# Kernel tuning notes

Hardware: AMD Instinct MI355X
Metric: run time of the kernel (lower is better)

## Reference

```python
import jax, jax.numpy as jnp
import numpy as np

N, F, H, C = 4096, 512, 8, 128
LEAKY_ALPHA = 0.2
MASK_VAL = -10e9  # spektral uses -10e9 * (1 - A)


def setup_inputs() -> dict:
    key = jax.random.key(0)
    k1, k2, k3, k4, k5 = jax.random.split(key, 5)
    X = jax.random.normal(k1, (N, F), dtype=jnp.float32)
    # sparse-ish binary adjacency with self loops (dense layout as the layer expects)
    A = (jax.random.uniform(k2, (N, N)) < 0.01).astype(jnp.float32)
    A = jnp.maximum(A, jnp.eye(N, dtype=jnp.float32))
    W = jax.random.normal(k3, (H, F, C), dtype=jnp.float32) * (1.0 / np.sqrt(F))
    a_self = jax.random.normal(k4, (H, C), dtype=jnp.float32) * (1.0 / np.sqrt(C))
    a_neigh = jax.random.normal(k5, (H, C), dtype=jnp.float32) * (1.0 / np.sqrt(C))
    bias = jnp.zeros((H, C), dtype=jnp.float32)
    return {"X": X, "A": A, "W": W, "a_self": a_self, "a_neigh": a_neigh, "bias": bias}


def reference(X, A, W, a_self, a_neigh, bias):
    # per-head feature projection: [H, N, C]
    feats = jnp.einsum("nf,hfc->hnc", X, W)
    # attention scores e_ij = LeakyReLU(a_self . h_i + a_neigh . h_j)
    s_self = jnp.einsum("hnc,hc->hn", feats, a_self)    # [H, N]
    s_neigh = jnp.einsum("hnc,hc->hn", feats, a_neigh)  # [H, N]
    dense = s_self[:, :, None] + s_neigh[:, None, :]    # [H, N, N]
    dense = jnp.where(dense > 0, dense, LEAKY_ALPHA * dense)
    # adjacency mask then row softmax (dropout_rate=0 -> identity)
    dense = dense + MASK_VAL * (1.0 - A)[None, :, :]
    coef = jax.nn.softmax(dense, axis=-1)               # [H, N, N]
    out = jnp.einsum("hnm,hmc->hnc", coef, feats)       # [H, N, C]
    out = out + bias[:, None, :]
    # concat heads: [N, H*C]
    out = jnp.transpose(out, (1, 0, 2)).reshape(N, H * C)
    return jax.nn.relu(out)
```

## Files before the change

kernel.cpp:

```cpp
#include <hip/hip_runtime.h>
#include <hip/hip_bf16.h>

#define GN 4096
#define GF 512
#define GH 8
#define GC 128
#define CAP 256
#define LCAP 128
#define XS 72

typedef __hip_bfloat16 bf16;
typedef unsigned short u16;
typedef unsigned int u32;
typedef __attribute__((ext_vector_type(8))) short bf16x8;
typedef __attribute__((ext_vector_type(4))) float f32x4;

static __device__ inline u16 f2u16(float x) {
    union { bf16 b; u16 u; } cv;
    cv.b = __float2bfloat16(x);
    return cv.u;
}

static __device__ inline float bf2f(short s) {
    return __uint_as_float((u32)(u16)s << 16);
}

__global__ __launch_bounds__(256) void prep_csr_kernel(
    const float* __restrict__ A, const float* __restrict__ X,
    const float* __restrict__ W, int* __restrict__ deg,
    u16* __restrict__ lists, u16* __restrict__ Xb, u16* __restrict__ WT)
{
    __shared__ u16 sT[16][520];
    int tid = threadIdx.x;
    int b   = blockIdx.x;

    if (b < 1024) {
        size_t idx = ((size_t)b * 256 + tid) * 8;
        float4 v0 = *(const float4*)(X + idx);
        float4 v1 = *(const float4*)(X + idx + 4);
        u16 o[8] = {f2u16(v0.x), f2u16(v0.y), f2u16(v0.z), f2u16(v0.w),
                    f2u16(v1.x), f2u16(v1.y), f2u16(v1.z), f2u16(v1.w)};
        *(bf16x8*)(Xb + idx) = *(bf16x8*)o;
        return;
    }
    if (b < 1088) {
        int wb = b - 1024;
        int h  = wb >> 3;
        int s16 = (wb & 7) * 16;
        const float* Wh = W + (size_t)h * GF * GC;
        for (int pass = 0; pass < 8; ++pass) {
            int k  = pass * 64 + (tid >> 2);
            int n4 = tid & 3;
            float4 v = *(const float4*)&Wh[(size_t)k * GC + s16 + n4 * 4];
            sT[n4 * 4 + 0][k] = f2u16(v.x);
            sT[n4 * 4 + 1][k] = f2u16(v.y);
            sT[n4 * 4 + 2][k] = f2u16(v.z);
            sT[n4 * 4 + 3][k] = f2u16(v.w);
        }
        __syncthreads();
        int n = tid >> 4, seg = tid & 15;
        u16* dst = WT + ((size_t)h * GC + s16 + n) * GF + seg * 32;
#pragma unroll
        for (int s = 0; s < 4; ++s)
            *(bf16x8*)(dst + s * 8) = *(const bf16x8*)&sT[n][seg * 32 + s * 8];
        return;
    }

    int i    = b - 1088;
    int lane = tid & 63;
    int* cnt = (int*)&sT[0][0];
    if (tid == 0) *cnt = 0;
    __syncthreads();

    u16* row = lists + (size_t)i * CAP;
    const float4* Arow = (const float4*)(A + (size_t)i * GN);
    unsigned long long ltmask = (lane == 63) ? ~0ull >> 1
                                             : (1ull << lane) - 1;

    float4 av[4];
#pragma unroll
    for (int it = 0; it < 4; ++it) av[it] = Arow[it * 256 + tid];

#pragma unroll
    for (int it = 0; it < 4; ++it) {
        float4 a = av[it];
        int j = (it * 256 + tid) * 4;
        bool f0 = a.x > 0.5f, f1 = a.y > 0.5f, f2 = a.z > 0.5f, f3 = a.w > 0.5f;
        unsigned long long m0 = __ballot(f0);
        unsigned long long m1 = __ballot(f1);
        unsigned long long m2 = __ballot(f2);
        unsigned long long m3 = __ballot(f3);
        int c0 = __popcll(m0), c1 = __popcll(m1), c2 = __popcll(m2);
        int tot = c0 + c1 + c2 + __popcll(m3);
        int base = 0;
        if (lane == 0 && tot) base = atomicAdd(cnt, tot);
        base = __shfl(base, 0);
        if (tot) {
            if (f0) {
                int s = base + __popcll(m0 & ltmask);
                if (s < CAP) row[s] = (u16)j;
            }
            if (f1) {
                int s = base + c0 + __popcll(m1 & ltmask);
                if (s < CAP) row[s] = (u16)(j + 1);
            }
            if (f2) {
                int s = base + c0 + c1 + __popcll(m2 & ltmask);
                if (s < CAP) row[s] = (u16)(j + 2);
            }
            if (f3) {
                int s = base + c0 + c1 + c2 + __popcll(m3 & ltmask);
                if (s < CAP) row[s] = (u16)(j + 3);
            }
        }
    }
    __syncthreads();
    if (tid == 0) deg[i] = *cnt < CAP ? *cnt : CAP;
}

__global__ __launch_bounds__(256) void feats_kernel(
    const u16* __restrict__ Xb, const u16* __restrict__ WT,
    const float* __restrict__ a_self, const float* __restrict__ a_neigh,
    u16* __restrict__ featsb, float* __restrict__ ssT,
    float* __restrict__ snT)
{
    __shared__ u16 sX[64 * XS];
    __shared__ u16 sW[128 * XS];

    int h   = blockIdx.x >> 6;
    int n0  = (blockIdx.x & 63) << 6;
    int tid = threadIdx.x;
    int lane = tid & 63, wv = tid >> 6;
    int lm = lane & 15, q = lane >> 4;

    const u16* Xp = Xb + (size_t)n0 * GF;
    const u16* Wp = WT + (size_t)h * GC * GF;

    uint4 xr[2], wr[4];

#define ISSUE_TILE(K0)                                                        \
    {                                                                         \
        _Pragma("unroll")                                                     \
        for (int it = 0; it < 2; ++it) {                                      \
            int idx = it * 256 + tid, row = idx >> 3, c = idx & 7;            \
            xr[it] = *(const uint4*)&Xp[(size_t)row * GF + (K0) + c * 8];     \
        }                                                                     \
        _Pragma("unroll")                                                     \
        for (int it = 0; it < 4; ++it) {                                      \
            int idx = it * 256 + tid, row = idx >> 3, c = idx & 7;            \
            wr[it] = *(const uint4*)&Wp[(size_t)row * GF + (K0) + c * 8];     \
        }                                                                     \
    }

#define STORE_TILE()                                                          \
    {                                                                         \
        _Pragma("unroll")                                                     \
        for (int it = 0; it < 2; ++it) {                                      \
            int idx = it * 256 + tid, row = idx >> 3, c = idx & 7;            \
            *(uint4*)&sX[row * XS + c * 8] = xr[it];                          \
        }                                                                     \
        _Pragma("unroll")                                                     \
        for (int it = 0; it < 4; ++it) {                                      \
            int idx = it * 256 + tid, row = idx >> 3, c = idx & 7;            \
            *(uint4*)&sW[row * XS + c * 8] = wr[it];                          \
        }                                                                     \
    }

    f32x4 acc[8];
#pragma unroll
    for (int nt = 0; nt < 8; ++nt) acc[nt] = (f32x4){0.f, 0.f, 0.f, 0.f};

    ISSUE_TILE(0)
    STORE_TILE()

    for (int k0 = 0; k0 < GF; k0 += 64) {
        __syncthreads();
        if (k0 + 64 < GF) ISSUE_TILE(k0 + 64)

#pragma unroll
        for (int ks = 0; ks < 64; ks += 32) {
            bf16x8 af = *(const bf16x8*)&sX[(wv * 16 + lm) * XS + ks + q * 8];
            bf16x8 bfr[8];
#pragma unroll
            for (int nt = 0; nt < 8; ++nt)
                bfr[nt] = *(const bf16x8*)&sW[(nt * 16 + lm) * XS + ks + q * 8];
#pragma unroll
            for (int nt = 0; nt < 8; ++nt)
                acc[nt] = __builtin_amdgcn_mfma_f32_16x16x32_bf16(
                    af, bfr[nt], acc[nt], 0, 0, 0);
        }
        __syncthreads();
        if (k0 + 64 < GF) STORE_TILE()
    }
#undef ISSUE_TILE
#undef STORE_TILE

    float aS[8], aN[8];
#pragma unroll
    for (int nt = 0; nt < 8; ++nt) {
        aS[nt] = a_self[h * GC + nt * 16 + lm];
        aN[nt] = a_neigh[h * GC + nt * 16 + lm];
    }
    float vs[4] = {0.f, 0.f, 0.f, 0.f};
    float vn[4] = {0.f, 0.f, 0.f, 0.f};
    int rbase = n0 + wv * 16 + q * 4;
    u16* fB = featsb + (size_t)(h >> 1) * GN * 256 + (h & 1) * 128;
#pragma unroll
    for (int nt = 0; nt < 8; ++nt) {
        f32x4 v = acc[nt];
        int col = nt * 16 + lm;
#pragma unroll
        for (int r = 0; r < 4; ++r) {
            fB[(size_t)(rbase + r) * 256 + col] = f2u16(v[r]);
            vs[r] += v[r] * aS[nt];
            vn[r] += v[r] * aN[nt];
        }
    }
#pragma unroll
    for (int r = 0; r < 4; ++r) {
        for (int off = 1; off < 16; off <<= 1) {
            vs[r] += __shfl_xor(vs[r], off);
            vn[r] += __shfl_xor(vn[r], off);
        }
        if (lm == 0) {
            ssT[(rbase + r) * GH + h] = vs[r];
            snT[(rbase + r) * GH + h] = vn[r];
        }
    }
}

__global__ __launch_bounds__(256) void attn_kernel(
    const int* __restrict__ deg, const u16* __restrict__ lists,
    const float* __restrict__ bias, const u16* __restrict__ featsb,
    const float* __restrict__ ssT, const float* __restrict__ snT,
    float* __restrict__ out)
{
    int tid  = threadIdx.x;
    int wv   = tid >> 6, lane = tid & 63;
    int bid  = blockIdx.x;
    int r8   = bid & 7;
    int hp   = r8 >> 1;
    int i    = (bid >> 3) * 8 + (r8 & 1) * 4 + wv;

    __shared__ float4 pjbuf[4][LCAP];
    float4* pj = pjbuf[wv];

    int M = deg[i];
    M = M < LCAP ? M : LCAP;
    const u16* row = lists + (size_t)i * CAP;

    float2 ssv = *(const float2*)&ssT[(size_t)i * GH + hp * 2];

    int ka = lane, kb = lane + 64;
    int ja = 0, jb = 0;
    float e0a = -1e30f, e1a = -1e30f, e0b = -1e30f, e1b = -1e30f;
    if (ka < M) {
        ja = row[ka];
        float2 sn = *(const float2*)&snT[(size_t)ja * GH + hp * 2];
        e0a = ssv.x + sn.x; e0a = e0a > 0.f ? e0a : 0.2f * e0a;
        e1a = ssv.y + sn.y; e1a = e1a > 0.f ? e1a : 0.2f * e1a;
    }
    if (kb < M) {
        jb = row[kb];
        float2 sn = *(const float2*)&snT[(size_t)jb * GH + hp * 2];
        e0b = ssv.x + sn.x; e0b = e0b > 0.f ? e0b : 0.2f * e0b;
        e1b = ssv.y + sn.y; e1b = e1b > 0.f ? e1b : 0.2f * e1b;
    }
    float m0 = fmaxf(e0a, e0b), m1 = fmaxf(e1a, e1b);
#pragma unroll
    for (int off = 32; off > 0; off >>= 1) {
        m0 = fmaxf(m0, __shfl_xor(m0, off));
        m1 = fmaxf(m1, __shfl_xor(m1, off));
    }

    float s0 = 0.f, s1 = 0.f;
    if (ka < M) {
        float p0 = __expf(e0a - m0), p1 = __expf(e1a - m1);
        pj[ka] = make_float4(p0, p1, __int_as_float(ja), 0.f);
        s0 += p0; s1 += p1;
    }
    if (kb < M) {
        float p0 = __expf(e0b - m0), p1 = __expf(e1b - m1);
        pj[kb] = make_float4(p0, p1, __int_as_float(jb), 0.f);
        s0 += p0; s1 += p1;
    }
#pragma unroll
    for (int off = 32; off > 0; off >>= 1) {
        s0 += __shfl_xor(s0, off);
        s1 += __shfl_xor(s1, off);
    }

    int par = lane >> 5;
    int cl  = lane & 31;
    float inv = (cl < 16) ? 1.f / s0 : 1.f / s1;

    const u16* fb = featsb + (size_t)hp * GN * 256 + cl * 8;
    float a0 = 0.f, a1 = 0.f, a2 = 0.f, a3 = 0.f;
    float a4 = 0.f, a5 = 0.f, a6 = 0.f, a7 = 0.f;

#define ACCUM(Q, WW)                                                          \
    {                                                                         \
        a0 += (WW) * bf2f((Q)[0]); a1 += (WW) * bf2f((Q)[1]);                 \
        a2 += (WW) * bf2f((Q)[2]); a3 += (WW) * bf2f((Q)[3]);                 \
        a4 += (WW) * bf2f((Q)[4]); a5 += (WW) * bf2f((Q)[5]);                 \
        a6 += (WW) * bf2f((Q)[6]); a7 += (WW) * bf2f((Q)[7]);                 \
    }

    int k = 0;
    for (; k + 8 <= M; k += 8) {
        float4 v0 = pj[k + par];
        float4 v1 = pj[k + 2 + par];
        float4 v2 = pj[k + 4 + par];
        float4 v3 = pj[k + 6 + par];
        int j0 = __float_as_int(v0.z), j1 = __float_as_int(v1.z);
        int j2 = __float_as_int(v2.z), j3 = __float_as_int(v3.z);
        bf16x8 q0 = *(const bf16x8*)(fb + (size_t)j0 * 256);
        bf16x8 q1 = *(const bf16x8*)(fb + (size_t)j1 * 256);
        bf16x8 q2 = *(const bf16x8*)(fb + (size_t)j2 * 256);
        bf16x8 q3 = *(const bf16x8*)(fb + (size_t)j3 * 256);
        float w0 = (cl < 16) ? v0.x : v0.y;
        float w1 = (cl < 16) ? v1.x : v1.y;
        float w2 = (cl < 16) ? v2.x : v2.y;
        float w3 = (cl < 16) ? v3.x : v3.y;
        ACCUM(q0, w0)
        ACCUM(q1, w1)
        ACCUM(q2, w2)
        ACCUM(q3, w3)
    }
    if (k + 4 <= M) {
        float4 v0 = pj[k + par], v1 = pj[k + 2 + par];
        int j0 = __float_as_int(v0.z), j1 = __float_as_int(v1.z);
        bf16x8 q0 = *(const bf16x8*)(fb + (size_t)j0 * 256);
        bf16x8 q1 = *(const bf16x8*)(fb + (size_t)j1 * 256);
        float w0 = (cl < 16) ? v0.x : v0.y;
        float w1 = (cl < 16) ? v1.x : v1.y;
        ACCUM(q0, w0)
        ACCUM(q1, w1)
        k += 4;
    }
    if (k + 2 <= M) {
        float4 v0 = pj[k + par];
        int j0 = __float_as_int(v0.z);
        bf16x8 q0 = *(const bf16x8*)(fb + (size_t)j0 * 256);
        float w0 = (cl < 16) ? v0.x : v0.y;
        ACCUM(q0, w0)
        k += 2;
    }
    if (k < M) {
        float4 v0 = pj[k];
        int j0 = __float_as_int(v0.z);
        bf16x8 q0 = *(const bf16x8*)(fb + (size_t)j0 * 256);
        float w0 = (cl < 16) ? v0.x : v0.y;
        if (par) w0 = 0.f;
        ACCUM(q0, w0)
    }
#undef ACCUM

    a0 += __shfl_xor(a0, 32); a1 += __shfl_xor(a1, 32);
    a2 += __shfl_xor(a2, 32); a3 += __shfl_xor(a3, 32);
    a4 += __shfl_xor(a4, 32); a5 += __shfl_xor(a5, 32);
    a6 += __shfl_xor(a6, 32); a7 += __shfl_xor(a7, 32);

    if (par == 0) {
        int co = hp * 256 + cl * 8;
        float4 b0 = *(const float4*)&bias[co];
        float4 b1 = *(const float4*)&bias[co + 4];
        float* op = out + (size_t)i * (GH * GC) + co;
        float4 o0, o1;
        o0.x = fmaxf(a0 * inv + b0.x, 0.f);
        o0.y = fmaxf(a1 * inv + b0.y, 0.f);
        o0.z = fmaxf(a2 * inv + b0.z, 0.f);
        o0.w = fmaxf(a3 * inv + b0.w, 0.f);
        o1.x = fmaxf(a4 * inv + b1.x, 0.f);
        o1.y = fmaxf(a5 * inv + b1.y, 0.f);
        o1.z = fmaxf(a6 * inv + b1.z, 0.f);
        o1.w = fmaxf(a7 * inv + b1.w, 0.f);
        *(float4*)op = o0;
        *(float4*)(op + 4) = o1;
    }
}

extern "C" void kernel_launch(void* const* d_in, const int* in_sizes, int n_in,
                              void* d_out, int out_size, void* d_ws, size_t ws_size,
                              hipStream_t stream)
{
    const float* X       = (const float*)d_in[0];
    const float* A       = (const float*)d_in[1];
    const float* W       = (const float*)d_in[2];
    const float* a_self  = (const float*)d_in[3];
    const float* a_neigh = (const float*)d_in[4];
    const float* bias    = (const float*)d_in[5];
    float* out = (float*)d_out;

    u16*   featsb = (u16*)d_ws;
    float* ssT    = (float*)(featsb + (size_t)GH * GN * GC);
    float* snT    = ssT + (size_t)GH * GN;
    int*   deg    = (int*)(snT + (size_t)GH * GN);
    u16*   lists  = (u16*)(deg + GN);
    u16*   Xb     = lists + (size_t)GN * CAP;
    u16*   WT     = Xb + (size_t)GN * GF;

    prep_csr_kernel<<<1088 + GN, 256, 0, stream>>>(A, X, W, deg, lists, Xb, WT);
    feats_kernel<<<GH * 64, 256, 0, stream>>>(Xb, WT, a_self, a_neigh,
                                              featsb, ssT, snT);
    attn_kernel<<<GH * GN / 8, 256, 0, stream>>>(deg, lists, bias, featsb,
                                                 ssT, snT, out);
}
```

Before: 164.3 us.

## Move adjacency CSR build into feats kernel to overlap with projection GEMM

The dense-adjacency scan that builds per-row neighbor lists moves out of the prep kernel and into the feature-projection launch as extra blocks after the 512 GEMM blocks. The prep kernel now only converts X and W to bf16. The memory-bound 64 MB adjacency read can then run at the same time as the compute-bound projection instead of before it. The cost is a larger combined grid with mixed block types, and the shared scratch is unified into one buffer.

```diff
diff --git a/kernel.cpp b/kernel.cpp
--- a/kernel.cpp
+++ b/kernel.cpp
@@ -25,10 +25,9 @@
     return __uint_as_float((u32)(u16)s << 16);
 }
 
-__global__ __launch_bounds__(256) void prep_csr_kernel(
-    const float* __restrict__ A, const float* __restrict__ X,
-    const float* __restrict__ W, int* __restrict__ deg,
-    u16* __restrict__ lists, u16* __restrict__ Xb, u16* __restrict__ WT)
+__global__ __launch_bounds__(256) void prep_kernel(
+    const float* __restrict__ X, const float* __restrict__ W,
+    u16* __restrict__ Xb, u16* __restrict__ WT)
 {
     __shared__ u16 sT[16][520];
     int tid = threadIdx.x;
@@ -43,93 +42,97 @@
         *(bf16x8*)(Xb + idx) = *(bf16x8*)o;
         return;
     }
-    if (b < 1088) {
-        int wb = b - 1024;
-        int h  = wb >> 3;
-        int s16 = (wb & 7) * 16;
-        const float* Wh = W + (size_t)h * GF * GC;
-        for (int pass = 0; pass < 8; ++pass) {
-            int k  = pass * 64 + (tid >> 2);
-            int n4 = tid & 3;
-            float4 v = *(const float4*)&Wh[(size_t)k * GC + s16 + n4 * 4];
-            sT[n4 * 4 + 0][k] = f2u16(v.x);
-            sT[n4 * 4 + 1][k] = f2u16(v.y);
-            sT[n4 * 4 + 2][k] = f2u16(v.z);
-            sT[n4 * 4 + 3][k] = f2u16(v.w);
+    int wb = b - 1024;
+    int h  = wb >> 3;
+    int s16 = (wb & 7) * 16;
+    const float* Wh = W + (size_t)h * GF * GC;
+    for (int pass = 0; pass < 8; ++pass) {
+        int k  = pass * 64 + (tid >> 2);
+        int n4 = tid & 3;
+        float4 v = *(const float4*)&Wh[(size_t)k * GC + s16 + n4 * 4];
+        sT[n4 * 4 + 0][k] = f2u16(v.x);
+        sT[n4 * 4 + 1][k] = f2u16(v.y);
+        sT[n4 * 4 + 2][k] = f2u16(v.z);
+        sT[n4 * 4 + 3][k] = f2u16(v.w);
+    }
+    __syncthreads();
+    int n = tid >> 4, seg = tid & 15;
+    u16* dst = WT + ((size_t)h * GC + s16 + n) * GF + seg * 32;
+#pragma unroll
+    for (int s = 0; s < 4; ++s)
+        *(bf16x8*)(dst + s * 8) = *(const bf16x8*)&sT[n][seg * 32 + s * 8];
+}
+
+__global__ __launch_bounds__(256) void feats_csr_kernel(
+    const u16* __restrict__ Xb, const u16* __restrict__ WT,
+    const float* __restrict__ a_self, const float* __restrict__ a_neigh,
+    const float* __restrict__ A, int* __restrict__ deg,
+    u16* __restrict__ lists, u16* __restrict__ featsb,
+    float* __restrict__ ssT, float* __restrict__ snT)
+{
+    __shared__ u16 smem[192 * XS];
+    int tid = threadIdx.x;
+    int b   = blockIdx.x;
+
+    if (b >= 512) {
+        int i    = b - 512;
+        int lane = tid & 63;
+        int* cnt = (int*)&smem[0];
+        if (tid == 0) *cnt = 0;
+        __syncthreads();
+
+        u16* row = lists + (size_t)i * CAP;
+        const float4* Arow = (const float4*)(A + (size_t)i * GN);
+        unsigned long long ltmask = (lane == 63) ? ~0ull >> 1
+                                                 : (1ull << lane) - 1;
+        float4 av[4];
+#pragma unroll
+        for (int it = 0; it < 4; ++it) av[it] = Arow[it * 256 + tid];
+
+#pragma unroll
+        for (int it = 0; it < 4; ++it) {
+            float4 a = av[it];
+            int j = (it * 256 + tid) * 4;
+            bool f0 = a.x > 0.5f, f1 = a.y > 0.5f;
+            bool f2 = a.z > 0.5f, f3 = a.w > 0.5f;
+            unsigned long long m0 = __ballot(f0);
+            unsigned long long m1 = __ballot(f1);
+            unsigned long long m2 = __ballot(f2);
+            unsigned long long m3 = __ballot(f3);
+            int c0 = __popcll(m0), c1 = __popcll(m1), c2 = __popcll(m2);
+            int tot = c0 + c1 + c2 + __popcll(m3);
+            int base = 0;
+            if (lane == 0 && tot) base = atomicAdd(cnt, tot);
+            base = __shfl(base, 0);
+            if (tot) {
+                if (f0) {
+                    int s = base + __popcll(m0 & ltmask);
+                    if (s < CAP) row[s] = (u16)j;
+                }
+                if (f1) {
+                    int s = base + c0 + __popcll(m1 & ltmask);
+                    if (s < CAP) row[s] = (u16)(j + 1);
+                }
+                if (f2) {
+                    int s = base + c0 + c1 + __popcll(m2 & ltmask);
+                    if (s < CAP) row[s] = (u16)(j + 2);
+                }
+                if (f3) {
+                    int s = base + c0 + c1 + c2 + __popcll(m3 & ltmask);
+                    if (s < CAP) row[s] = (u16)(j + 3);
+                }
+            }
         }
         __syncthreads();
-        int n = tid >> 4, seg = tid & 15;
-        u16* dst = WT + ((size_t)h * GC + s16 + n) * GF + seg * 32;
-#pragma unroll
-        for (int s = 0; s < 4; ++s)
-            *(bf16x8*)(dst + s * 8) = *(const bf16x8*)&sT[n][seg * 32 + s * 8];
+        if (tid == 0) deg[i] = *cnt < CAP ? *cnt : CAP;
         return;
     }
 
-    int i    = b - 1088;
-    int lane = tid & 63;
-    int* cnt = (int*)&sT[0][0];
-    if (tid == 0) *cnt = 0;
-    __syncthreads();
-
-    u16* row = lists + (size_t)i * CAP;
-    const float4* Arow = (const float4*)(A + (size_t)i * GN);
-    unsigned long long ltmask = (lane == 63) ? ~0ull >> 1
-                                             : (1ull << lane) - 1;
-
-    float4 av[4];
-#pragma unroll
-    for (int it = 0; it < 4; ++it) av[it] = Arow[it * 256 + tid];
-
-#pragma unroll
-    for (int it = 0; it < 4; ++it) {
-        float4 a = av[it];
-        int j = (it * 256 + tid) * 4;
-        bool f0 = a.x > 0.5f, f1 = a.y > 0.5f, f2 = a.z > 0.5f, f3 = a.w > 0.5f;
-        unsigned long long m0 = __ballot(f0);
-        unsigned long long m1 = __ballot(f1);
-        unsigned long long m2 = __ballot(f2);
-        unsigned long long m3 = __ballot(f3);
-        int c0 = __popcll(m0), c1 = __popcll(m1), c2 = __popcll(m2);
-        int tot = c0 + c1 + c2 + __popcll(m3);
-        int base = 0;
-        if (lane == 0 && tot) base = atomicAdd(cnt, tot);
-        base = __shfl(base, 0);
-        if (tot) {
-            if (f0) {
-                int s = base + __popcll(m0 & ltmask);
-                if (s < CAP) row[s] = (u16)j;
-            }
-            if (f1) {
-                int s = base + c0 + __popcll(m1 & ltmask);
-                if (s < CAP) row[s] = (u16)(j + 1);
-            }
-            if (f2) {
-                int s = base + c0 + c1 + __popcll(m2 & ltmask);
-                if (s < CAP) row[s] = (u16)(j + 2);
-            }
-            if (f3) {
-                int s = base + c0 + c1 + c2 + __popcll(m3 & ltmask);
-                if (s < CAP) row[s] = (u16)(j + 3);
-            }
-        }
-    }
-    __syncthreads();
-    if (tid == 0) deg[i] = *cnt < CAP ? *cnt : CAP;
-}
-
-__global__ __launch_bounds__(256) void feats_kernel(
-    const u16* __restrict__ Xb, const u16* __restrict__ WT,
-    const float* __restrict__ a_self, const float* __restrict__ a_neigh,
-    u16* __restrict__ featsb, float* __restrict__ ssT,
-    float* __restrict__ snT)
-{
-    __shared__ u16 sX[64 * XS];
-    __shared__ u16 sW[128 * XS];
-
-    int h   = blockIdx.x >> 6;
-    int n0  = (blockIdx.x & 63) << 6;
-    int tid = threadIdx.x;
+    u16* sX = smem;
+    u16* sW = smem + 64 * XS;
+
+    int h   = b >> 6;
+    int n0  = (b & 63) << 6;
     int lane = tid & 63, wv = tid >> 6;
     int lm = lane & 15, q = lane >> 4;
 
@@ -400,9 +403,10 @@
     u16*   Xb     = lists + (size_t)GN * CAP;
     u16*   WT     = Xb + (size_t)GN * GF;
 
-    prep_csr_kernel<<<1088 + GN, 256, 0, stream>>>(A, X, W, deg, lists, Xb, WT);
-    feats_kernel<<<GH * 64, 256, 0, stream>>>(Xb, WT, a_self, a_neigh,
-                                              featsb, ssT, snT);
+    prep_kernel<<<1088, 256, 0, stream>>>(X, W, Xb, WT);
+    feats_csr_kernel<<<512 + GN, 256, 0, stream>>>(Xb, WT, a_self, a_neigh,
+                                                   A, deg, lists, featsb,
+                                                   ssT, snT);
     attn_kernel<<<GH * GN / 8, 256, 0, stream>>>(deg, lists, bias, featsb,
                                                  ssT, snT, out);
 }
```

Measured after the change: 166.9 us. Within noise of the previous version (+1.6%).
